# Performance work log

Measured on AMD Instinct MI355X. Metric: run time of the kernel, lower is better.

## Reference

```python
import jax, jax.numpy as jnp
import numpy as np

HID = 64
NH = 4
DH = 16  # head dim
SEQ = 25  # 5x5 grid
LN_EPS = 1e-5
COS_EPS = 1e-8
TOP_K = 5


def _ln(x, g, b):
    m = x.mean(-1, keepdims=True)
    v = ((x - m) ** 2).mean(-1, keepdims=True)
    return (x - m) / jnp.sqrt(v + LN_EPS) * g + b


def _encoder_layer(x, Wqkv, bqkv, Wo, bo, g1, be1, W1, b1, W2, b2, g2, be2):
    # post-norm TransformerEncoderLayer (norm_first=False), relu FFN, dropout=eval(off)
    B, S, D = x.shape
    qkv = x @ Wqkv.T + bqkv                      # [B,S,3D]
    q, k, v = jnp.split(qkv, 3, axis=-1)
    q = q.reshape(B, S, NH, DH)
    k = k.reshape(B, S, NH, DH)
    v = v.reshape(B, S, NH, DH)
    att = jax.nn.softmax(jnp.einsum('bqhd,bkhd->bhqk', q, k) / jnp.sqrt(jnp.float32(DH)), axis=-1)
    o = jnp.einsum('bhqk,bkhd->bqhd', att, v).reshape(B, S, D)
    o = o @ Wo.T + bo
    x = _ln(x + o, g1, be1)
    f = jax.nn.relu(x @ W1.T + b1) @ W2.T + b2
    return _ln(x + f, g2, be2)


def setup_inputs() -> dict:
    key = jax.random.key(0)
    ks = jax.random.split(key, 16)
    B = 16384
    d = {}
    d['input_grid'] = jax.random.normal(ks[0], (B, 10, 5, 5), dtype=jnp.float32)
    d['pos_embed'] = jax.random.normal(ks[1], (SEQ, HID), dtype=jnp.float32)
    d['color_emb'] = jax.random.normal(ks[2], (10, HID), dtype=jnp.float32)
    # 2 transformer layers, params stacked on leading axis
    d['Wqkv'] = jax.random.normal(ks[3], (2, 3 * HID, HID), dtype=jnp.float32) * 0.02
    d['bqkv'] = jnp.zeros((2, 3 * HID), jnp.float32)
    d['Wo'] = jax.random.normal(ks[4], (2, HID, HID), dtype=jnp.float32) * 0.02
    d['bo'] = jnp.zeros((2, HID), jnp.float32)
    d['ln1_g'] = jnp.ones((2, HID), jnp.float32)
    d['ln1_b'] = jnp.zeros((2, HID), jnp.float32)
    d['W1'] = jax.random.normal(ks[5], (2, 2 * HID, HID), dtype=jnp.float32) * 0.02
    d['b1'] = jnp.zeros((2, 2 * HID), jnp.float32)
    d['W2'] = jax.random.normal(ks[6], (2, HID, 2 * HID), dtype=jnp.float32) * 0.02
    d['b2'] = jnp.zeros((2, HID), jnp.float32)
    d['ln2_g'] = jnp.ones((2, HID), jnp.float32)
    d['ln2_b'] = jnp.zeros((2, HID), jnp.float32)
    d['pattern_memory'] = jax.random.normal(ks[7], (100, SEQ * HID), dtype=jnp.float32)
    d['hW1'] = jax.random.normal(ks[8], (HID, HID), dtype=jnp.float32) * 0.02
    d['hb1'] = jnp.zeros((HID,), jnp.float32)
    d['hW2'] = jax.random.normal(ks[9], (10, HID), dtype=jnp.float32) * 0.02
    d['hb2'] = jnp.zeros((10,), jnp.float32)
    return d


def reference(input_grid, pos_embed, color_emb, Wqkv, bqkv, Wo, bo, ln1_g, ln1_b,
              W1, b1, W2, b2, ln2_g, ln2_b, pattern_memory, hW1, hb1, hW2, hb2):
    B, C, H, W = input_grid.shape
    S = H * W
    idx = jnp.argmax(input_grid, axis=1).reshape(B, S)      # [B,S] int
    x = color_emb[idx] + pos_embed[None, :S]                # [B,S,64]
    for l in range(2):
        x = _encoder_layer(x, Wqkv[l], bqkv[l], Wo[l], bo[l], ln1_g[l], ln1_b[l],
                           W1[l], b1[l], W2[l], b2[l], ln2_g[l], ln2_b[l])
    x_flat = x.reshape(B, S * HID)                          # [B,1600]
    xn = x_flat / jnp.maximum(jnp.linalg.norm(x_flat, axis=1, keepdims=True), COS_EPS)
    pn = pattern_memory / jnp.maximum(jnp.linalg.norm(pattern_memory, axis=1, keepdims=True), COS_EPS)
    scores = xn @ pn.T                                      # [B,100] cosine sims
    top_s, top_i = jax.lax.top_k(scores, TOP_K)             # [B,5]
    top_p = pattern_memory[top_i]                           # [B,5,1600]
    w = jax.nn.softmax(top_s, axis=1)[..., None]            # [B,5,1]
    pattern_influence = (top_p * w).sum(axis=1).reshape(B, S, HID)
    x = x + 0.5 * pattern_influence
    out = jax.nn.relu(x @ hW1.T + hb1) @ hW2.T + hb2        # [B,S,10]
    return out.reshape(B, H, W, 10).transpose(0, 3, 1, 2)   # [B,10,H,W]
```

## Files before the change

kernel.cpp:

```cpp
#include <hip/hip_runtime.h>
#include <cstdint>

#define IPB 10

__device__ __forceinline__ float dot64r(const float (&xr)[64], const float* __restrict__ w){
  float a0=0.f,a1=0.f,a2=0.f,a3=0.f;
  #pragma unroll
  for (int d=0; d<64; d+=4){
    a0 = fmaf(xr[d  ], w[d  ], a0);
    a1 = fmaf(xr[d+1], w[d+1], a1);
    a2 = fmaf(xr[d+2], w[d+2], a2);
    a3 = fmaf(xr[d+3], w[d+3], a3);
  }
  return (a0+a1)+(a2+a3);
}

__device__ __forceinline__ void ln64(float (&v)[64], const float* __restrict__ g, const float* __restrict__ b){
  float s0=0.f,s1=0.f,s2=0.f,s3=0.f;
  #pragma unroll
  for (int d=0; d<64; d+=4){ s0+=v[d]; s1+=v[d+1]; s2+=v[d+2]; s3+=v[d+3]; }
  float m = ((s0+s1)+(s2+s3)) * 0.015625f;
  s0=s1=s2=s3=0.f;
  #pragma unroll
  for (int d=0; d<64; d+=4){
    float t0=v[d]-m, t1=v[d+1]-m, t2=v[d+2]-m, t3=v[d+3]-m;
    s0=fmaf(t0,t0,s0); s1=fmaf(t1,t1,s1); s2=fmaf(t2,t2,s2); s3=fmaf(t3,t3,s3);
  }
  float var = ((s0+s1)+(s2+s3)) * 0.015625f;
  float inv = 1.0f / sqrtf(var + 1e-5f);
  #pragma unroll
  for (int d=0; d<64; d++) v[d] = fmaf((v[d]-m)*inv, g[d], b[d]);
}

__global__ void kPinv(const float* __restrict__ pm, float* __restrict__ pinv){
  __shared__ float red[256];
  int p = blockIdx.x, tid = threadIdx.x;
  float ss = 0.f;
  for (int k = tid; k < 1600; k += 256){ float v = pm[(size_t)p*1600 + k]; ss = fmaf(v,v,ss); }
  red[tid] = ss; __syncthreads();
  for (int w = 128; w > 0; w >>= 1){ if (tid < w) red[tid] += red[tid+w]; __syncthreads(); }
  if (tid == 0) pinv[p] = 1.0f / fmaxf(sqrtf(red[0]), 1e-8f);
}

__global__ void kTbl(const float* __restrict__ pos, const float* __restrict__ cemb,
                     const float* __restrict__ Wqkv, const float* __restrict__ bqkv,
                     float* __restrict__ tbl){
  __shared__ float e[64];
  int sc = blockIdx.x;
  int s = sc / 10, c = sc - s*10;
  int j = threadIdx.x;
  if (j < 64) e[j] = cemb[c*64 + j] + pos[s*64 + j];
  __syncthreads();
  const float* w = Wqkv + (size_t)j*64;
  float a0=0.f,a1=0.f,a2=0.f,a3=0.f;
  #pragma unroll
  for (int d=0; d<64; d+=4){
    a0 = fmaf(e[d  ], w[d  ], a0);
    a1 = fmaf(e[d+1], w[d+1], a1);
    a2 = fmaf(e[d+2], w[d+2], a2);
    a3 = fmaf(e[d+3], w[d+3], a3);
  }
  tbl[(size_t)sc*192 + j] = ((a0+a1)+(a2+a3)) + bqkv[j];
}

__global__ __launch_bounds__(256,1) void kT(
  const float* __restrict__ gridin, const float* __restrict__ cemb, const float* __restrict__ pos,
  const float* __restrict__ Wqkv, const float* __restrict__ bqkv,
  const float* __restrict__ Wo,   const float* __restrict__ bo,
  const float* __restrict__ g1,   const float* __restrict__ be1,
  const float* __restrict__ W1,   const float* __restrict__ b1,
  const float* __restrict__ W2,   const float* __restrict__ b2,
  const float* __restrict__ g2,   const float* __restrict__ be2,
  const float* __restrict__ tbl,  float* __restrict__ xws, float* __restrict__ xinv, int B)
{
  __shared__ float smem[12256];
  float* kl   = smem;
  float* vlds = smem + 4000;
  float* ql   = smem + 8000;
  float* sh16 = smem;
  float* red  = smem + 12000;

  const int tid = threadIdx.x;
  const int r = tid;
  const int i = r / 25;
  const int s = r - i*25;
  const int gi = blockIdx.x * IPB + i;
  const bool act = (r < 250) && (gi < B);

  int am = 0;
  float x[64];
  if (act){
    const float* gp = gridin + (size_t)gi*250 + s;
    float mx = gp[0];
    #pragma unroll
    for (int c=1;c<10;c++){ float v = gp[c*25]; if (v > mx){ mx = v; am = c; } }
    const float4* ce = (const float4*)(cemb + am*64);
    const float4* pe = (const float4*)(pos  + s*64);
    #pragma unroll
    for (int u=0;u<16;u++){
      float4 a = ce[u], bb = pe[u];
      x[4*u+0]=a.x+bb.x; x[4*u+1]=a.y+bb.y; x[4*u+2]=a.z+bb.z; x[4*u+3]=a.w+bb.w;
    }
  }

  for (int l=0; l<2; l++){
    __syncthreads();
    float o[64];
    #pragma unroll
    for (int d=0;d<64;d++) o[d]=0.f;

    #pragma unroll
    for (int h=0; h<4; h++){
      float q[16];
      if (act){
        if (l == 0){
          const float* tr = tbl + (size_t)(s*10+am)*192 + h*16;
          #pragma unroll
          for (int u=0;u<4;u++){
            float4 a = ((const float4*)tr)[u];
            q[4*u]=a.x; q[4*u+1]=a.y; q[4*u+2]=a.z; q[4*u+3]=a.w;
            ((float4*)(kl   + r*16))[u] = ((const float4*)(tr+64 ))[u];
            ((float4*)(vlds + r*16))[u] = ((const float4*)(tr+128))[u];
          }
        } else {
          #pragma unroll 1
          for (int jj=0;jj<16;jj++){
            const int row = h*16 + jj;
            const float* wq = Wqkv + (size_t)(192 + row)*64;
            const float* wk = Wqkv + (size_t)(192 + 64 + row)*64;
            const float* wv = Wqkv + (size_t)(192 + 128 + row)*64;
            ql[r*16+jj]   = dot64r(x, wq) + bqkv[192+row];
            kl[r*16+jj]   = dot64r(x, wk) + bqkv[192+64+row];
            vlds[r*16+jj] = dot64r(x, wv) + bqkv[192+128+row];
          }
        }
      }
      __syncthreads();
      if (act){
        if (l != 0){
          #pragma unroll
          for (int u=0;u<4;u++){
            float4 a = ((const float4*)(ql + r*16))[u];
            q[4*u]=a.x; q[4*u+1]=a.y; q[4*u+2]=a.z; q[4*u+3]=a.w;
          }
        }
        float att[25];
        float mx = -3.402823466e38f;
        #pragma unroll
        for (int kk=0;kk<25;kk++){
          const float4* kr = (const float4*)(kl + (i*25+kk)*16);
          float4 A=kr[0], Bq=kr[1], C=kr[2], D=kr[3];
          float p0 = q[0]*A.x,  p1 = q[1]*A.y,  p2 = q[2]*A.z,  p3 = q[3]*A.w;
          p0 = fmaf(q[4], Bq.x, p0); p1 = fmaf(q[5], Bq.y, p1); p2 = fmaf(q[6], Bq.z, p2); p3 = fmaf(q[7], Bq.w, p3);
          p0 = fmaf(q[8], C.x,  p0); p1 = fmaf(q[9], C.y,  p1); p2 = fmaf(q[10],C.z,  p2); p3 = fmaf(q[11],C.w,  p3);
          p0 = fmaf(q[12],D.x,  p0); p1 = fmaf(q[13],D.y,  p1); p2 = fmaf(q[14],D.z,  p2); p3 = fmaf(q[15],D.w,  p3);
          float v = ((p0+p1)+(p2+p3)) * 0.25f;
          att[kk] = v; mx = fmaxf(mx, v);
        }
        float ssum = 0.f;
        #pragma unroll
        for (int kk=0;kk<25;kk++){ float e = __expf(att[kk]-mx); att[kk]=e; ssum += e; }
        float rs = 1.0f / ssum;
        #pragma unroll
        for (int kk=0;kk<25;kk++){
          float a = att[kk]*rs;
          const float4* vr = (const float4*)(vlds + (i*25+kk)*16);
          float4 A=vr[0], Bq=vr[1], C=vr[2], D=vr[3];
          o[h*16+ 0]=fmaf(a,A.x ,o[h*16+ 0]); o[h*16+ 1]=fmaf(a,A.y ,o[h*16+ 1]);
          o[h*16+ 2]=fmaf(a,A.z ,o[h*16+ 2]); o[h*16+ 3]=fmaf(a,A.w ,o[h*16+ 3]);
          o[h*16+ 4]=fmaf(a,Bq.x,o[h*16+ 4]); o[h*16+ 5]=fmaf(a,Bq.y,o[h*16+ 5]);
          o[h*16+ 6]=fmaf(a,Bq.z,o[h*16+ 6]); o[h*16+ 7]=fmaf(a,Bq.w,o[h*16+ 7]);
          o[h*16+ 8]=fmaf(a,C.x ,o[h*16+ 8]); o[h*16+ 9]=fmaf(a,C.y ,o[h*16+ 9]);
          o[h*16+10]=fmaf(a,C.z ,o[h*16+10]); o[h*16+11]=fmaf(a,C.w ,o[h*16+11]);
          o[h*16+12]=fmaf(a,D.x ,o[h*16+12]); o[h*16+13]=fmaf(a,D.y ,o[h*16+13]);
          o[h*16+14]=fmaf(a,D.z ,o[h*16+14]); o[h*16+15]=fmaf(a,D.w ,o[h*16+15]);
        }
      }
      __syncthreads();
    }

    if (act){
      #pragma unroll
      for (int t=0;t<4;t++){
        #pragma unroll 1
        for (int jj=0;jj<16;jj++){
          const int j = t*16 + jj;
          const float* wr = Wo + (size_t)(l*64 + j)*64;
          sh16[r*18 + jj] = dot64r(o, wr) + bo[l*64+j];
        }
        #pragma unroll
        for (int u=0;u<8;u++){
          float2 a = *(const float2*)(sh16 + r*18 + 2*u);
          x[t*16 + 2*u] += a.x; x[t*16 + 2*u + 1] += a.y;
        }
      }
      ln64(x, g1 + l*64, be1 + l*64);
    }
    __syncthreads();

    if (act){
      float fa[64];
      #pragma unroll
      for (int j=0;j<64;j++) fa[j] = b2[l*64+j];
      #pragma unroll 1
      for (int t=0;t<8;t++){
        #pragma unroll 1
        for (int jj=0;jj<16;jj++){
          const float* wr = W1 + (size_t)(l*128 + t*16 + jj)*64;
          sh16[r*18 + jj] = fmaxf(dot64r(x, wr) + b1[l*128 + t*16 + jj], 0.f);
        }
        float f1s[16];
        #pragma unroll
        for (int u=0;u<8;u++){
          float2 a = *(const float2*)(sh16 + r*18 + 2*u);
          f1s[2*u]=a.x; f1s[2*u+1]=a.y;
        }
        #pragma unroll
        for (int j=0;j<64;j++){
          const float* wr = W2 + (size_t)(l*64 + j)*128 + t*16;
          float a0 = f1s[0]*wr[0];
          float a1 = f1s[1]*wr[1];
          float a2 = f1s[2]*wr[2];
          float a3 = f1s[3]*wr[3];
          a0 = fmaf(f1s[ 4], wr[ 4], a0); a1 = fmaf(f1s[ 5], wr[ 5], a1);
          a2 = fmaf(f1s[ 6], wr[ 6], a2); a3 = fmaf(f1s[ 7], wr[ 7], a3);
          a0 = fmaf(f1s[ 8], wr[ 8], a0); a1 = fmaf(f1s[ 9], wr[ 9], a1);
          a2 = fmaf(f1s[10], wr[10], a2); a3 = fmaf(f1s[11], wr[11], a3);
          a0 = fmaf(f1s[12], wr[12], a0); a1 = fmaf(f1s[13], wr[13], a1);
          a2 = fmaf(f1s[14], wr[14], a2); a3 = fmaf(f1s[15], wr[15], a3);
          fa[j] += ((a0+a1)+(a2+a3));
        }
      }
      #pragma unroll
      for (int j=0;j<64;j++) x[j] += fa[j];
      ln64(x, g2 + l*64, be2 + l*64);
    }
  }

  float ss = 0.f;
  if (act){
    float4* xo = (float4*)(xws + (size_t)(gi*25 + s)*64);
    float s0=0.f,s1=0.f,s2=0.f,s3=0.f;
    #pragma unroll
    for (int u=0;u<16;u++){
      float4 a; a.x=x[4*u]; a.y=x[4*u+1]; a.z=x[4*u+2]; a.w=x[4*u+3];
      xo[u] = a;
      s0=fmaf(a.x,a.x,s0); s1=fmaf(a.y,a.y,s1); s2=fmaf(a.z,a.z,s2); s3=fmaf(a.w,a.w,s3);
    }
    ss = (s0+s1)+(s2+s3);
  }
  __syncthreads();
  red[tid] = ss;
  __syncthreads();
  if (tid < IPB){
    int g = blockIdx.x*IPB + tid;
    if (g < B){
      float t = 0.f;
      #pragma unroll
      for (int u=0;u<25;u++) t += red[tid*25+u];
      xinv[g] = 1.0f / fmaxf(sqrtf(t), 1e-8f);
    }
  }
}

__global__ __launch_bounds__(256,4) void kS(const float* __restrict__ xws, const float* __restrict__ xinv,
    const float* __restrict__ pm, const float* __restrict__ pinv, float* __restrict__ scr, int B){
  __shared__ float xt[64*36];
  __shared__ float pt[112*36];
  const int tid = threadIdx.x;
  const int pg = tid & 15, ig = tid >> 4;
  const int it0 = blockIdx.x * 64;
  float acc[4][7];
  #pragma unroll
  for (int a=0;a<4;a++)
    #pragma unroll
    for (int c=0;c<7;c++) acc[a][c] = 0.f;

  for (int k0 = 0; k0 < 1600; k0 += 32){
    __syncthreads();
    #pragma unroll
    for (int jj=0;jj<2;jj++){
      int cch = tid + jj*256;
      int row = cch >> 3, kc = cch & 7;
      int it = it0 + row; if (it >= B) it = B-1;
      *(float4*)(xt + row*36 + kc*4) = *(const float4*)(xws + (size_t)it*1600 + k0 + kc*4);
    }
    #pragma unroll
    for (int jj=0;jj<4;jj++){
      int cch = tid + jj*256;
      if (cch < 896){
        int row = cch >> 3, kc = cch & 7;
        float4 v;
        if (row < 100) v = *(const float4*)(pm + (size_t)row*1600 + k0 + kc*4);
        else { v.x=0.f; v.y=0.f; v.z=0.f; v.w=0.f; }
        *(float4*)(pt + row*36 + kc*4) = v;
      }
    }
    __syncthreads();
    #pragma unroll
    for (int k=0;k<32;k+=4){
      float4 xv[4], pv[7];
      #pragma unroll
      for (int a=0;a<4;a++) xv[a] = *(const float4*)(xt + (ig*4+a)*36 + k);
      #pragma unroll
      for (int c=0;c<7;c++) pv[c] = *(const float4*)(pt + (pg+16*c)*36 + k);
      #pragma unroll
      for (int a=0;a<4;a++)
        #pragma unroll
        for (int c=0;c<7;c++){
          float t = acc[a][c];
          t = fmaf(xv[a].x, pv[c].x, t);
          t = fmaf(xv[a].y, pv[c].y, t);
          t = fmaf(xv[a].z, pv[c].z, t);
          t = fmaf(xv[a].w, pv[c].w, t);
          acc[a][c] = t;
        }
    }
  }
  #pragma unroll
  for (int a=0;a<4;a++){
    int it = it0 + ig*4 + a;
    if (it < B){
      float xi = xinv[it];
      #pragma unroll
      for (int c=0;c<7;c++){
        int p = pg + 16*c;
        if (p < 100) scr[(size_t)it*100 + p] = acc[a][c] * xi * pinv[p];
      }
    }
  }
}

__global__ __launch_bounds__(256,2) void kH(const float* __restrict__ xws, const float* __restrict__ scr,
   const float* __restrict__ pm, const float* __restrict__ hW1, const float* __restrict__ hb1,
   const float* __restrict__ hW2, const float* __restrict__ hb2, float* __restrict__ outp, int B){
  __shared__ float hls[16500];
  __shared__ int   tI[IPB*5];
  __shared__ float tW[IPB*5];
  const int tid = threadIdx.x;

  if (tid < IPB){
    int g = blockIdx.x*IPB + tid;
    if (g < B){
      const float* sc = scr + (size_t)g*100;
      float v0=-3.402823466e38f,v1=v0,v2=v0,v3=v0,v4=v0;
      int j0=0,j1=0,j2=0,j3=0,j4=0;
      for (int p=0;p<100;p++){
        float v = sc[p];
        if (v > v4){
          if (v > v2){
            if (v > v1){
              if (v > v0){ v4=v3;j4=j3; v3=v2;j3=j2; v2=v1;j2=j1; v1=v0;j1=j0; v0=v;j0=p; }
              else       { v4=v3;j4=j3; v3=v2;j3=j2; v2=v1;j2=j1; v1=v; j1=p; }
            } else       { v4=v3;j4=j3; v3=v2;j3=j2; v2=v; j2=p; }
          } else {
            if (v > v3)  { v4=v3;j4=j3; v3=v; j3=p; }
            else         { v4=v; j4=p; }
          }
        }
      }
      float e1=__expf(v1-v0), e2=__expf(v2-v0), e3=__expf(v3-v0), e4=__expf(v4-v0);
      float inv = 1.0f/(1.0f+e1+e2+e3+e4);
      tI[tid*5+0]=j0; tI[tid*5+1]=j1; tI[tid*5+2]=j2; tI[tid*5+3]=j3; tI[tid*5+4]=j4;
      tW[tid*5+0]=inv; tW[tid*5+1]=e1*inv; tW[tid*5+2]=e2*inv; tW[tid*5+3]=e3*inv; tW[tid*5+4]=e4*inv;
    }
  }
  __syncthreads();

  const int r = tid;
  const int i = r/25, s = r - i*25;
  const int gi = blockIdx.x*IPB + i;
  if (r < 250 && gi < B){
    float x[64];
    const float4* xi4 = (const float4*)(xws + (size_t)(gi*25+s)*64);
    #pragma unroll
    for (int u=0;u<16;u++){ float4 a = xi4[u]; x[4*u]=a.x; x[4*u+1]=a.y; x[4*u+2]=a.z; x[4*u+3]=a.w; }
    #pragma unroll
    for (int t=0;t<5;t++){
      float w = 0.5f * tW[i*5+t];
      const float4* pr = (const float4*)(pm + (size_t)tI[i*5+t]*1600 + s*64);
      #pragma unroll
      for (int u=0;u<16;u++){
        float4 a = pr[u];
        x[4*u  ]=fmaf(w,a.x,x[4*u  ]); x[4*u+1]=fmaf(w,a.y,x[4*u+1]);
        x[4*u+2]=fmaf(w,a.z,x[4*u+2]); x[4*u+3]=fmaf(w,a.w,x[4*u+3]);
      }
    }
    #pragma unroll 1
    for (int j=0;j<64;j++){
      hls[r*66+j] = fmaxf(dot64r(x, hW1 + (size_t)j*64) + hb1[j], 0.f);
    }
    float hreg[64];
    #pragma unroll
    for (int u=0;u<32;u++){ float2 a = *(const float2*)(hls + r*66 + 2*u); hreg[2*u]=a.x; hreg[2*u+1]=a.y; }
    #pragma unroll 1
    for (int c=0;c<10;c++){
      outp[(size_t)gi*250 + c*25 + s] = dot64r(hreg, hW2 + (size_t)c*64) + hb2[c];
    }
  }
}

extern "C" void kernel_launch(void* const* d_in, const int* in_sizes, int n_in,
                              void* d_out, int out_size, void* d_ws, size_t ws_size,
                              hipStream_t stream){
  (void)n_in; (void)out_size; (void)ws_size;
  const float* gridin = (const float*)d_in[0];
  const float* pos    = (const float*)d_in[1];
  const float* cemb   = (const float*)d_in[2];
  const float* Wqkv   = (const float*)d_in[3];
  const float* bqkv   = (const float*)d_in[4];
  const float* Wo     = (const float*)d_in[5];
  const float* bo     = (const float*)d_in[6];
  const float* g1     = (const float*)d_in[7];
  const float* be1    = (const float*)d_in[8];
  const float* W1     = (const float*)d_in[9];
  const float* b1     = (const float*)d_in[10];
  const float* W2     = (const float*)d_in[11];
  const float* b2     = (const float*)d_in[12];
  const float* g2     = (const float*)d_in[13];
  const float* be2    = (const float*)d_in[14];
  const float* pm     = (const float*)d_in[15];
  const float* hW1    = (const float*)d_in[16];
  const float* hb1    = (const float*)d_in[17];
  const float* hW2    = (const float*)d_in[18];
  const float* hb2    = (const float*)d_in[19];
  float* outp = (float*)d_out;
  const int B = in_sizes[0] / 250;

  float* ws    = (float*)d_ws;
  float* tbl   = ws;
  float* pinv  = ws + 48000;
  float* xws   = ws + 48128;
  float* xinv  = xws + (size_t)B*1600;
  float* scr   = xinv + B;

  kPinv<<<100, 256, 0, stream>>>(pm, pinv);
  kTbl <<<250, 192, 0, stream>>>(pos, cemb, Wqkv, bqkv, tbl);
  kT   <<<(B + IPB - 1)/IPB, 256, 0, stream>>>(gridin, cemb, pos, Wqkv, bqkv, Wo, bo,
                                               g1, be1, W1, b1, W2, b2, g2, be2,
                                               tbl, xws, xinv, B);
  kS   <<<(B + 63)/64, 256, 0, stream>>>(xws, xinv, pm, pinv, scr, B);
  kH   <<<(B + IPB - 1)/IPB, 256, 0, stream>>>(xws, scr, pm, hW1, hb1, hW2, hb2, outp, B);
}
```

Measured before the change: 3.254 ms.

## Stage layer weights in shared memory and allow two blocks per CU

Cooperatively copies the layer-1 QKV weights (per head), the Wo matrix, and W1/W2 chunks into a new LDS buffer. Each thread then reads them with float4 LDS broadcast loads instead of per-thread global or scalar loads. Launch bounds change from 1 to 2 blocks per CU to raise occupancy. The cost is extra barriers and LDS traffic. Halving the register budget per thread also risks spills given the large per-thread x/o/fa arrays.

New measurement: 3.158 ms. 3.0% less time.

```diff
diff --git a/kernel.cpp b/kernel.cpp
--- a/kernel.cpp
+++ b/kernel.cpp
@@ -15,6 +15,19 @@
   return (a0+a1)+(a2+a3);
 }
 
+__device__ __forceinline__ float dot64s(const float (&xr)[64], const float* w){
+  float a0=0.f,a1=0.f,a2=0.f,a3=0.f;
+  #pragma unroll
+  for (int d=0; d<64; d+=4){
+    float4 wv = *(const float4*)(w + d);
+    a0 = fmaf(xr[d  ], wv.x, a0);
+    a1 = fmaf(xr[d+1], wv.y, a1);
+    a2 = fmaf(xr[d+2], wv.z, a2);
+    a3 = fmaf(xr[d+3], wv.w, a3);
+  }
+  return (a0+a1)+(a2+a3);
+}
+
 __device__ __forceinline__ void ln64(float (&v)[64], const float* __restrict__ g, const float* __restrict__ b){
   float s0=0.f,s1=0.f,s2=0.f,s3=0.f;
   #pragma unroll
@@ -30,6 +43,22 @@
   float inv = 1.0f / sqrtf(var + 1e-5f);
   #pragma unroll
   for (int d=0; d<64; d++) v[d] = fmaf((v[d]-m)*inv, g[d], b[d]);
+}
+
+__device__ __forceinline__ void stage_rows64(float* dst, const float* __restrict__ src, int nrows, int tid){
+  const int total = nrows*16;
+  for (int idx = tid; idx < total; idx += 256){
+    int rr = idx >> 4, c4 = idx & 15;
+    *(float4*)(dst + rr*64 + c4*4) = *(const float4*)(src + (size_t)rr*64 + c4*4);
+  }
+}
+__device__ __forceinline__ void stage_w2(float* dst, const float* __restrict__ src, int tid){
+  #pragma unroll
+  for (int p=0;p<2;p++){
+    int idx = tid + p*256;
+    int rr = idx >> 3, c4 = idx & 7;
+    *(float4*)(dst + rr*32 + c4*4) = *(const float4*)(src + (size_t)rr*128 + c4*4);
+  }
 }
 
 __global__ void kPinv(const float* __restrict__ pm, float* __restrict__ pinv){
@@ -63,7 +92,7 @@
   tbl[(size_t)sc*192 + j] = ((a0+a1)+(a2+a3)) + bqkv[j];
 }
 
-__global__ __launch_bounds__(256,1) void kT(
+__global__ __launch_bounds__(256,2) void kT(
   const float* __restrict__ gridin, const float* __restrict__ cemb, const float* __restrict__ pos,
   const float* __restrict__ Wqkv, const float* __restrict__ bqkv,
   const float* __restrict__ Wo,   const float* __restrict__ bo,
@@ -73,12 +102,14 @@
   const float* __restrict__ g2,   const float* __restrict__ be2,
   const float* __restrict__ tbl,  float* __restrict__ xws, float* __restrict__ xinv, int B)
 {
-  __shared__ float smem[12256];
+  __shared__ float smem[16352];
   float* kl   = smem;
   float* vlds = smem + 4000;
   float* ql   = smem + 8000;
   float* sh16 = smem;
   float* red  = smem + 12000;
+  float* wbuf = smem + 12256;
+  float* wbuf2= wbuf + 2048;
 
   const int tid = threadIdx.x;
   const int r = tid;
@@ -111,6 +142,13 @@
 
     #pragma unroll
     for (int h=0; h<4; h++){
+      if (l == 1){
+        __syncthreads();
+        stage_rows64(wbuf,        Wqkv + (size_t)(192       + h*16)*64, 16, tid);
+        stage_rows64(wbuf + 1024, Wqkv + (size_t)(192 + 64  + h*16)*64, 16, tid);
+        stage_rows64(wbuf + 2048, Wqkv + (size_t)(192 + 128 + h*16)*64, 16, tid);
+        __syncthreads();
+      }
       float q[16];
       if (act){
         if (l == 0){
@@ -126,12 +164,9 @@
           #pragma unroll 1
           for (int jj=0;jj<16;jj++){
             const int row = h*16 + jj;
-            const float* wq = Wqkv + (size_t)(192 + row)*64;
-            const float* wk = Wqkv + (size_t)(192 + 64 + row)*64;
-            const float* wv = Wqkv + (size_t)(192 + 128 + row)*64;
-            ql[r*16+jj]   = dot64r(x, wq) + bqkv[192+row];
-            kl[r*16+jj]   = dot64r(x, wk) + bqkv[192+64+row];
-            vlds[r*16+jj] = dot64r(x, wv) + bqkv[192+128+row];
+            ql[r*16+jj]   = dot64s(x, wbuf +        jj*64) + bqkv[192+row];
+            kl[r*16+jj]   = dot64s(x, wbuf + 1024 + jj*64) + bqkv[192+64+row];
+            vlds[r*16+jj] = dot64s(x, wbuf + 2048 + jj*64) + bqkv[192+128+row];
           }
         }
       }
@@ -179,14 +214,15 @@
       __syncthreads();
     }
 
+    stage_rows64(wbuf, Wo + (size_t)l*64*64, 64, tid);
+    __syncthreads();
     if (act){
       #pragma unroll
       for (int t=0;t<4;t++){
         #pragma unroll 1
         for (int jj=0;jj<16;jj++){
           const int j = t*16 + jj;
-          const float* wr = Wo + (size_t)(l*64 + j)*64;
-          sh16[r*18 + jj] = dot64r(o, wr) + bo[l*64+j];
+          sh16[r*18 + jj] = dot64s(o, wbuf + j*64) + bo[l*64+j];
         }
         #pragma unroll
         for (int u=0;u<8;u++){
@@ -198,16 +234,24 @@
     }
     __syncthreads();
 
+    float fa[64];
     if (act){
-      float fa[64];
       #pragma unroll
       for (int j=0;j<64;j++) fa[j] = b2[l*64+j];
-      #pragma unroll 1
-      for (int t=0;t<8;t++){
+    }
+    #pragma unroll 1
+    for (int t=0;t<8;t++){
+      if ((t & 1) == 0){
+        __syncthreads();
+        stage_rows64(wbuf, W1 + (size_t)(l*128 + t*16)*64, 32, tid);
+        stage_w2(wbuf2, W2 + (size_t)l*64*128 + t*16, tid);
+        __syncthreads();
+      }
+      if (act){
+        const int half = (t & 1) * 16;
         #pragma unroll 1
         for (int jj=0;jj<16;jj++){
-          const float* wr = W1 + (size_t)(l*128 + t*16 + jj)*64;
-          sh16[r*18 + jj] = fmaxf(dot64r(x, wr) + b1[l*128 + t*16 + jj], 0.f);
+          sh16[r*18 + jj] = fmaxf(dot64s(x, wbuf + (half+jj)*64) + b1[l*128 + t*16 + jj], 0.f);
         }
         float f1s[16];
         #pragma unroll
@@ -217,20 +261,26 @@
         }
         #pragma unroll
         for (int j=0;j<64;j++){
-          const float* wr = W2 + (size_t)(l*64 + j)*128 + t*16;
-          float a0 = f1s[0]*wr[0];
-          float a1 = f1s[1]*wr[1];
-          float a2 = f1s[2]*wr[2];
-          float a3 = f1s[3]*wr[3];
-          a0 = fmaf(f1s[ 4], wr[ 4], a0); a1 = fmaf(f1s[ 5], wr[ 5], a1);
-          a2 = fmaf(f1s[ 6], wr[ 6], a2); a3 = fmaf(f1s[ 7], wr[ 7], a3);
-          a0 = fmaf(f1s[ 8], wr[ 8], a0); a1 = fmaf(f1s[ 9], wr[ 9], a1);
-          a2 = fmaf(f1s[10], wr[10], a2); a3 = fmaf(f1s[11], wr[11], a3);
-          a0 = fmaf(f1s[12], wr[12], a0); a1 = fmaf(f1s[13], wr[13], a1);
-          a2 = fmaf(f1s[14], wr[14], a2); a3 = fmaf(f1s[15], wr[15], a3);
+          const float* wr = wbuf2 + j*32 + half;
+          float4 A = *(const float4*)(wr);
+          float4 Bv = *(const float4*)(wr+4);
+          float4 C = *(const float4*)(wr+8);
+          float4 D = *(const float4*)(wr+12);
+          float a0 = f1s[0]*A.x;
+          float a1 = f1s[1]*A.y;
+          float a2 = f1s[2]*A.z;
+          float a3 = f1s[3]*A.w;
+          a0 = fmaf(f1s[ 4], Bv.x, a0); a1 = fmaf(f1s[ 5], Bv.y, a1);
+          a2 = fmaf(f1s[ 6], Bv.z, a2); a3 = fmaf(f1s[ 7], Bv.w, a3);
+          a0 = fmaf(f1s[ 8], C.x,  a0); a1 = fmaf(f1s[ 9], C.y,  a1);
+          a2 = fmaf(f1s[10], C.z,  a2); a3 = fmaf(f1s[11], C.w,  a3);
+          a0 = fmaf(f1s[12], D.x,  a0); a1 = fmaf(f1s[13], D.y,  a1);
+          a2 = fmaf(f1s[14], D.z,  a2); a3 = fmaf(f1s[15], D.w,  a3);
           fa[j] += ((a0+a1)+(a2+a3));
         }
       }
+    }
+    if (act){
       #pragma unroll
       for (int j=0;j<64;j++) x[j] += fa[j];
       ln64(x, g2 + l*64, be2 + l*64);
```
